# Kernel tuning notes

Measured on AMD Instinct MI355X. Metric: run time of the kernel, lower is better.

The kernel has to match this reference:

```python
import jax, jax.numpy as jnp
import numpy as np

GRID_SIZE = 100
N_GREEN = 524288
N_RED = 524288
LATENT_DIM = 10
HIDDEN = 128
IN_DIM = LATENT_DIM + 3 + 1  # z + level_data + loop index
TEMPERATURE = 500.0


def setup_inputs() -> dict:
    key = jax.random.key(0)
    ks = jax.random.split(key, 13)
    def lin(k, out_d, in_d):
        kw, kb = jax.random.split(k)
        s = 1.0 / np.sqrt(in_d)
        W = jax.random.uniform(kw, (out_d, in_d), jnp.float32, -s, s)
        b = jax.random.uniform(kb, (out_d,), jnp.float32, -s, s)
        return W, b
    z = jax.random.normal(ks[0], (LATENT_DIM,), jnp.float32)
    level_data = jnp.array([GRID_SIZE, N_GREEN, N_RED], dtype=jnp.int64)
    gW1, gb1 = lin(ks[1], HIDDEN, IN_DIM)
    gW2, gb2 = lin(ks[2], HIDDEN, HIDDEN)
    gW3, gb3 = lin(ks[3], 1, HIDDEN)
    rW1, rb1 = lin(ks[4], HIDDEN, IN_DIM)
    rW2, rb2 = lin(ks[5], HIDDEN, HIDDEN)
    rW3, rb3 = lin(ks[6], 1, HIDDEN)
    return {
        'z': z, 'level_data': level_data,
        'gW1': gW1, 'gb1': gb1, 'gW2': gW2, 'gb2': gb2, 'gW3': gW3, 'gb3': gb3,
        'rW1': rW1, 'rb1': rb1, 'rW2': rW2, 'rb2': rb2, 'rW3': rW3, 'rb3': rb3,
    }


def _mlp(x, W1, b1, W2, b2, W3, b3):
    # Linear -> LeakyReLU(0.2) -> Linear -> ELU(alpha=1) -> Linear
    h = jax.nn.leaky_relu(x @ W1.T + b1, negative_slope=0.2)
    h = jax.nn.elu(h @ W2.T + b2, alpha=1.0)
    return h @ W3.T + b3  # [N, 1]


def _coords(z_ext, n, W1, b1, W2, b2, W3, b3, scale):
    # batch all loop indices 0..n-1 into one GEMM call instead of n tiny launches
    idx = jnp.arange(n, dtype=jnp.float32)[:, None]            # [n, 1]
    x = jnp.concatenate(
        [jnp.broadcast_to(z_ext, (n, z_ext.shape[0])), idx], axis=1)  # [n, 14]
    out = _mlp(x, W1, b1, W2, b2, W3, b3)[:, 0]                 # [n]
    return (jax.nn.sigmoid(out / TEMPERATURE) * scale).astype(jnp.int32)


def reference(z, level_data, gW1, gb1, gW2, gb2, gW3, gb3,
              rW1, rb1, rW2, rb2, rW3, rb3):
    scale = level_data[0].astype(jnp.float32) ** 2 - 1.0  # grid_size^2 - 1
    z_ext = jnp.concatenate([z, level_data.astype(jnp.float32)])  # [13]
    coords_green = _coords(z_ext, N_GREEN, gW1, gb1, gW2, gb2, gW3, gb3, scale)
    coords_red = _coords(z_ext, N_RED, rW1, rb1, rW2, rb2, rW3, rb3, scale)
    return coords_green, coords_red
```

## Files before the change

kernel.cpp:

```cpp
#include <hip/hip_runtime.h>
#include <hip/hip_bf16.h>
#include <math.h>


#define HIDDEN 128
#define REGIONS 129
#define NEVT 512
#define CDSTRIDE (NEVT + 8)
#define WS_HDR 16
#define STS(g)      (WS_HDR + (g)*HIDDEN)
#define TIMES_OFF   (WS_HDR + 2*HIDDEN)
#define TIMES(g,r)  (TIMES_OFF + ((g)*REGIONS + (r))*NEVT)
#define CTAB_OFF    (TIMES_OFF + 2*REGIONS*NEVT)
#define CTAB(g,r)   (CTAB_OFF + ((g)*REGIONS + (r))*CDSTRIDE)
#define DTAB_OFF    (CTAB_OFF + 2*REGIONS*CDSTRIDE)
#define DTAB(g,r)   (DTAB_OFF + ((g)*REGIONS + (r))*CDSTRIDE)

__device__ __constant__ float TH[4] = {-4.f, -1.8f, -0.7f, 0.f};
__device__ __constant__ float PM[5] = {0.f, 0.0668106f, 0.3011695f, 0.7191639f, 1.f};
__device__ __constant__ float PQ[5] = {-1.f, -0.7144420f, -0.2925961f, 0.f, 0.f};

__global__ __launch_bounds__(512) void build_kernel(
    const float* __restrict__ z, const int* __restrict__ level,
    const float* __restrict__ gW1, const float* __restrict__ gb1,
    const float* __restrict__ gW2, const float* __restrict__ gb2,
    const float* __restrict__ gW3, const float* __restrict__ gb3,
    const float* __restrict__ rW1, const float* __restrict__ rb1,
    const float* __restrict__ rW2, const float* __restrict__ rb2,
    const float* __restrict__ rW3, const float* __restrict__ rb3,
    float* __restrict__ ws, int N)
{
    int g = blockIdx.x / REGIONS;
    int r = blockIdx.x - g * REGIONS;
    const float* W1 = g ? rW1 : gW1;  const float* b1 = g ? rb1 : gb1;
    const float* W2 = g ? rW2 : gW2;  const float* b2 = g ? rb2 : gb2;
    const float* W3 = g ? rW3 : gW3;  const float* b3 = g ? rb3 : gb3;

    __shared__ float zext[16];
    __shared__ float cs[HIDDEN], wv[HIDDEN], tb_l[HIDDEN], sts[HIDDEN];
    __shared__ float sc[HIDDEN], sw[HIDDEN], al[HIDDEN], be[HIDDEN];
    __shared__ float pa[4][HIDDEN], pb[4][HIDDEN];
    __shared__ float ev_t[NEVT], ev_c[NEVT], ev_d[NEVT];
    __shared__ float so_t[NEVT], so_c[NEVT], so_d[NEVT];
    __shared__ float pc_[NEVT], pd_[NEVT];
    __shared__ float c0s, d0s;
    __shared__ int cnt;
    int t = threadIdx.x;

    if (t == 0) {
        int g0 = level[0], l1 = level[1], l2 = level[2];
        if (l1 == 0) { l1 = level[2]; l2 = level[4]; }
        zext[10] = (float)g0; zext[11] = (float)l1; zext[12] = (float)l2;
        cnt = 0;
        if (blockIdx.x == 0) ws[0] = (float)g0 * (float)g0 - 1.0f;
    }
    if (t < 10) zext[t] = z[t];
    __syncthreads();

    if (t < HIDDEN) {
        float c = b1[t];
        #pragma unroll
        for (int q = 0; q < 13; ++q) c = fmaf(W1[t * 14 + q], zext[q], c);
        float w = W1[t * 14 + 13];
        cs[t] = c; wv[t] = w;
        float Nf = (float)N, tb = -c / w;
        if (!(tb > 0.0f)) tb = 0.0f;
        if (!(tb < Nf))  tb = Nf;
        tb_l[t] = tb;
    }
    __syncthreads();
    if (t < HIDDEN) {
        float tb = tb_l[t]; int rk = 0;
        for (int k = 0; k < HIDDEN; ++k) {
            float tk = tb_l[k];
            rk += (tk < tb || (tk == tb && k < t)) ? 1 : 0;
        }
        sts[rk] = tb;
        if (r == 0) ws[STS(g) + rk] = tb;
    }
    __syncthreads();
    float i0 = (r == 0) ? 0.0f : sts[r - 1];
    float i1 = (r == REGIONS - 1) ? (float)N : sts[r];

    if (t < HIDDEN) {
        float c = cs[t], w = wv[t];
        float mid = 0.5f * (i0 + i1);
        float s = (fmaf(mid, w, c) > 0.0f) ? 1.0f : 0.2f;
        sc[t] = s * c;  sw[t] = s * w;
    }
    __syncthreads();

    {
        int k = t & 127, q = t >> 7;
        float a = 0.0f, bb = 0.0f;
        const float4* row4 = (const float4*)(W2 + k * HIDDEN + q * 32);
        #pragma unroll
        for (int j4 = 0; j4 < 8; ++j4) {
            float4 w2 = row4[j4]; int j = q * 32 + j4 * 4;
            a = fmaf(w2.x, sc[j+0], a);  bb = fmaf(w2.x, sw[j+0], bb);
            a = fmaf(w2.y, sc[j+1], a);  bb = fmaf(w2.y, sw[j+1], bb);
            a = fmaf(w2.z, sc[j+2], a);  bb = fmaf(w2.z, sw[j+2], bb);
            a = fmaf(w2.w, sc[j+3], a);  bb = fmaf(w2.w, sw[j+3], bb);
        }
        pa[q][k] = a;  pb[q][k] = bb;
    }
    __syncthreads();
    if (t < HIDDEN) {
        al[t] = pa[0][t] + pa[1][t] + pa[2][t] + pa[3][t] + b2[t];
        be[t] = pb[0][t] + pb[1][t] + pb[2][t] + pb[3][t];
    }
    __syncthreads();

    {
        int ku = t >> 2, h = t & 3;
        float a = al[ku], b = be[ku], w3 = W3[ku];
        float p0 = fmaf(i0, b, a);
        int pcq = (p0 >= TH[0]) + (p0 >= TH[1]) + (p0 >= TH[2]) + (p0 >= TH[3]);
        bool up = (b > 0.0f), dn = (b < 0.0f);
        bool dir_ok = up ? (h >= pcq) : (dn && (h < pcq));
        float tc = (TH[h] - a) / b;
        if (dir_ok && (tc <= i1)) {
            float dm, dq;
            if (up) { dm = PM[h+1] - PM[h]; dq = PQ[h+1] - PQ[h]; }
            else    { dm = PM[h] - PM[h+1]; dq = PQ[h] - PQ[h+1]; }
            int pos = atomicAdd(&cnt, 1);
            ev_t[pos] = tc;
            ev_c[pos] = w3 * fmaf(dm, a, dq);
            ev_d[pos] = w3 * dm * b;
        }
    }
    if (t < HIDDEN) {
        float a = al[t], b = be[t], w3 = W3[t];
        float p0 = fmaf(i0, b, a);
        int pp = (p0 >= TH[0]) + (p0 >= TH[1]) + (p0 >= TH[2]) + (p0 >= TH[3]);
        pa[0][t] = w3 * fmaf(PM[pp], a, PQ[pp]);
        pb[0][t] = w3 * PM[pp] * b;
    }
    __syncthreads();
    int m = cnt;

    if (t < 64) {
        float sA = pa[0][t] + pa[0][t + 64];
        float sB = pb[0][t] + pb[0][t + 64];
        #pragma unroll
        for (int off = 32; off >= 1; off >>= 1) {
            sA += __shfl_down(sA, off);
            sB += __shfl_down(sB, off);
        }
        if (t == 0) { c0s = sA + b3[0]; d0s = sB; }
    }
    if (t < m) {
        float myt = ev_t[t]; int rk = 0;
        for (int e = 0; e < m; ++e) {
            float te = ev_t[e];
            rk += (te < myt || (te == myt && e < t)) ? 1 : 0;
        }
        so_t[rk] = myt;  so_c[rk] = ev_c[t];  so_d[rk] = ev_d[t];
    }
    __syncthreads();
    if (t < m) {
        float vc = 0.0f, vd = 0.0f;
        for (int e = 0; e <= t; ++e) { vc += so_c[e]; vd += so_d[e]; }
        pc_[t] = vc;  pd_[t] = vd;
    }
    __syncthreads();

    float C0 = c0s, D0 = d0s;
    float totc = (m > 0) ? pc_[m - 1] : 0.0f;
    float totd = (m > 0) ? pd_[m - 1] : 0.0f;
    float* Tt = ws + TIMES(g, r);
    float* Tc = ws + CTAB(g, r);
    float* Td = ws + DTAB(g, r);
    Tt[t]     = (t < m) ? so_t[t] : INFINITY;
    Tc[t + 1] = C0 + ((t < m) ? pc_[t] : totc);
    Td[t + 1] = D0 + ((t < m) ? pd_[t] : totd);
    if (t == 0) { Tc[0] = C0; Td[0] = D0; }
}

__device__ __forceinline__ void seg_lookup(
    const float* __restrict__ ws, const float* __restrict__ lts,
    int g, float fi, int& r, int& a)
{
    int lo = 0, hi = HIDDEN;
    #pragma unroll
    for (int s = 0; s < 7; ++s) { int mm = (lo + hi) >> 1; if (lts[mm] <= fi) lo = mm + 1; else hi = mm; }
    r = lo;
    const float* Tt = ws + TIMES(g, r);
    int aa = 0, bb = NEVT;
    #pragma unroll
    for (int s = 0; s < 9; ++s) { int mm = (aa + bb) >> 1; if (Tt[mm] <= fi) aa = mm + 1; else bb = mm; }
    a = aa;
}

__global__ __launch_bounds__(256) void gen_kernel(
    const float* __restrict__ ws, int* __restrict__ out, int N, int total)
{
    __shared__ float lts[HIDDEN];
    __shared__ float uC, uD, uScale;
    __shared__ int ra[2];
    int tid = threadIdx.x;
    int e0 = blockIdx.x * 256;
    int g = (e0 >= N) ? 1 : 0;
    int e = e0 + tid;
    if (tid < HIDDEN) lts[tid] = ws[STS(g) + tid];
    if (tid == 0) uScale = ws[0];
    __syncthreads();

    float fi = (float)(e - g * N);
    if (tid < 2) {
        float fq = (float)((tid == 0 ? e0 : e0 + 255) - g * N);
        int rr, aa; seg_lookup(ws, lts, g, fq, rr, aa);
        ra[tid] = (rr << 16) | aa;
        if (tid == 0) { uC = ws[CTAB(g, rr) + aa]; uD = ws[DTAB(g, rr) + aa]; }
    }
    __syncthreads();

    float C, D;
    if (ra[0] == ra[1]) {
        C = uC; D = uD;
    } else {
        int rr, aa; seg_lookup(ws, lts, g, fi, rr, aa);
        C = ws[CTAB(g, rr) + aa];
        D = ws[DTAB(g, rr) + aa];
    }
    float o = fmaf(fi, D, C);
    float sg = 1.0f / (1.0f + __expf(-o * (1.0f / 500.0f)));
    if (e < total) out[e] = (int)(sg * uScale);
}

extern "C" void kernel_launch(void* const* d_in, const int* in_sizes, int n_in,
                              void* d_out, int out_size, void* d_ws, size_t ws_size,
                              hipStream_t stream) {
    const float* z   = (const float*)d_in[0];
    const int* level = (const int*)d_in[1];
    const float* gW1 = (const float*)d_in[2];
    const float* gb1 = (const float*)d_in[3];
    const float* gW2 = (const float*)d_in[4];
    const float* gb2 = (const float*)d_in[5];
    const float* gW3 = (const float*)d_in[6];
    const float* gb3 = (const float*)d_in[7];
    const float* rW1 = (const float*)d_in[8];
    const float* rb1 = (const float*)d_in[9];
    const float* rW2 = (const float*)d_in[10];
    const float* rb2 = (const float*)d_in[11];
    const float* rW3 = (const float*)d_in[12];
    const float* rb3 = (const float*)d_in[13];
    int* out  = (int*)d_out;
    float* ws = (float*)d_ws;
    int N = out_size / 2;

    build_kernel<<<2 * REGIONS, 512, 0, stream>>>(z, level,
        gW1, gb1, gW2, gb2, gW3, gb3, rW1, rb1, rW2, rb2, rW3, rb3, ws, N);
    gen_kernel<<<(out_size + 255) / 256, 256, 0, stream>>>(ws, out, N, out_size);
}
```

Measured before the change: 97.28 us.

## Replace per-element binary search with chunk directory and vectorized sequential scan

The build kernel now writes a directory that maps each 128-element chunk to its starting region and event index, plus each region's end time. The gen kernel reads this directory entry and then advances linearly through events while producing four outputs per thread with an int4 store. This removes the two binary searches per element and the shared-memory setup in the gen kernel. The per-region prefix sum becomes a serial loop on one thread, and building the directory adds an O(m) count per chunk in the build kernel, which may lengthen it. The int4 store assumes the total output size is a multiple of four.

```diff
diff --git a/kernel.cpp b/kernel.cpp
--- a/kernel.cpp
+++ b/kernel.cpp
@@ -7,14 +7,17 @@
 #define REGIONS 129
 #define NEVT 512
 #define CDSTRIDE (NEVT + 8)
+#define CHUNK_SH 7
 #define WS_HDR 16
-#define STS(g)      (WS_HDR + (g)*HIDDEN)
-#define TIMES_OFF   (WS_HDR + 2*HIDDEN)
+#define TIMES_OFF   (WS_HDR)
 #define TIMES(g,r)  (TIMES_OFF + ((g)*REGIONS + (r))*NEVT)
 #define CTAB_OFF    (TIMES_OFF + 2*REGIONS*NEVT)
 #define CTAB(g,r)   (CTAB_OFF + ((g)*REGIONS + (r))*CDSTRIDE)
 #define DTAB_OFF    (CTAB_OFF + 2*REGIONS*CDSTRIDE)
 #define DTAB(g,r)   (DTAB_OFF + ((g)*REGIONS + (r))*CDSTRIDE)
+#define RTS_OFF     (DTAB_OFF + 2*REGIONS*CDSTRIDE)
+#define RTS(g)      (RTS_OFF + (g)*REGIONS)
+#define DIR_OFF     (RTS_OFF + 2*REGIONS + 16)
 
 __device__ __constant__ float TH[4] = {-4.f, -1.8f, -0.7f, 0.f};
 __device__ __constant__ float PM[5] = {0.f, 0.0668106f, 0.3011695f, 0.7191639f, 1.f};
@@ -28,7 +31,7 @@
     const float* __restrict__ rW1, const float* __restrict__ rb1,
     const float* __restrict__ rW2, const float* __restrict__ rb2,
     const float* __restrict__ rW3, const float* __restrict__ rb3,
-    float* __restrict__ ws, int N)
+    float* __restrict__ ws, int* __restrict__ dir, int N, int nchunk)
 {
     int g = blockIdx.x / REGIONS;
     int r = blockIdx.x - g * REGIONS;
@@ -41,8 +44,7 @@
     __shared__ float sc[HIDDEN], sw[HIDDEN], al[HIDDEN], be[HIDDEN];
     __shared__ float pa[4][HIDDEN], pb[4][HIDDEN];
     __shared__ float ev_t[NEVT], ev_c[NEVT], ev_d[NEVT];
-    __shared__ float so_t[NEVT], so_c[NEVT], so_d[NEVT];
-    __shared__ float pc_[NEVT], pd_[NEVT];
+    __shared__ float so_t[NEVT], pc_[NEVT], pd_[NEVT];
     __shared__ float c0s, d0s;
     __shared__ int cnt;
     int t = threadIdx.x;
@@ -76,11 +78,11 @@
             rk += (tk < tb || (tk == tb && k < t)) ? 1 : 0;
         }
         sts[rk] = tb;
-        if (r == 0) ws[STS(g) + rk] = tb;
     }
     __syncthreads();
     float i0 = (r == 0) ? 0.0f : sts[r - 1];
     float i1 = (r == REGIONS - 1) ? (float)N : sts[r];
+    if (t == 0) ws[RTS(g) + r] = i1;
 
     if (t < HIDDEN) {
         float c = cs[t], w = wv[t];
@@ -155,13 +157,12 @@
             float te = ev_t[e];
             rk += (te < myt || (te == myt && e < t)) ? 1 : 0;
         }
-        so_t[rk] = myt;  so_c[rk] = ev_c[t];  so_d[rk] = ev_d[t];
-    }
-    __syncthreads();
-    if (t < m) {
+        so_t[rk] = myt;  pc_[rk] = ev_c[t];  pd_[rk] = ev_d[t];
+    }
+    __syncthreads();
+    if (t == 0) {
         float vc = 0.0f, vd = 0.0f;
-        for (int e = 0; e <= t; ++e) { vc += so_c[e]; vd += so_d[e]; }
-        pc_[t] = vc;  pd_[t] = vd;
+        for (int e = 0; e < m; ++e) { vc += pc_[e]; vd += pd_[e]; pc_[e] = vc; pd_[e] = vd; }
     }
     __syncthreads();
 
@@ -175,57 +176,56 @@
     Tc[t + 1] = C0 + ((t < m) ? pc_[t] : totc);
     Td[t + 1] = D0 + ((t < m) ? pd_[t] : totd);
     if (t == 0) { Tc[0] = C0; Td[0] = D0; }
+
+    int qlo = ((int)i0) >> CHUNK_SH;
+    for (int q = qlo + t; ; q += 512) {
+        float fc = (float)(q << CHUNK_SH);
+        if (!(fc < i1)) break;
+        if (fc >= i0 && q < nchunk) {
+            int a = 0;
+            for (int e = 0; e < m; ++e) a += (so_t[e] <= fc) ? 1 : 0;
+            dir[g * nchunk + q] = (r << 16) | a;
+        }
+    }
 }
 
-__device__ __forceinline__ void seg_lookup(
-    const float* __restrict__ ws, const float* __restrict__ lts,
-    int g, float fi, int& r, int& a)
+__global__ __launch_bounds__(256) void gen_kernel(
+    const float* __restrict__ ws, const int* __restrict__ dir,
+    int* __restrict__ out, int N, int total, int nchunk)
 {
-    int lo = 0, hi = HIDDEN;
+    int e0 = (blockIdx.x * 256 + threadIdx.x) * 4;
+    if (e0 >= total) return;
+    int g = (e0 >= N) ? 1 : 0;
+    int i = e0 - g * N;
+
+    int pd = dir[g * nchunk + (i >> CHUNK_SH)];
+    int r = pd >> 16, a = pd & 0xffff;
+    const float* Tt = ws + TIMES(g, r);
+    const float* Tc = ws + CTAB(g, r);
+    const float* Td = ws + DTAB(g, r);
+    const float* RT = ws + RTS(g);
+    float rtEnd = RT[r];
+    float nextT = Tt[a];
+    float C = Tc[a], D = Td[a];
+    float scale = ws[0];
+
+    int4 res;
     #pragma unroll
-    for (int s = 0; s < 7; ++s) { int mm = (lo + hi) >> 1; if (lts[mm] <= fi) lo = mm + 1; else hi = mm; }
-    r = lo;
-    const float* Tt = ws + TIMES(g, r);
-    int aa = 0, bb = NEVT;
-    #pragma unroll
-    for (int s = 0; s < 9; ++s) { int mm = (aa + bb) >> 1; if (Tt[mm] <= fi) aa = mm + 1; else bb = mm; }
-    a = aa;
-}
-
-__global__ __launch_bounds__(256) void gen_kernel(
-    const float* __restrict__ ws, int* __restrict__ out, int N, int total)
-{
-    __shared__ float lts[HIDDEN];
-    __shared__ float uC, uD, uScale;
-    __shared__ int ra[2];
-    int tid = threadIdx.x;
-    int e0 = blockIdx.x * 256;
-    int g = (e0 >= N) ? 1 : 0;
-    int e = e0 + tid;
-    if (tid < HIDDEN) lts[tid] = ws[STS(g) + tid];
-    if (tid == 0) uScale = ws[0];
-    __syncthreads();
-
-    float fi = (float)(e - g * N);
-    if (tid < 2) {
-        float fq = (float)((tid == 0 ? e0 : e0 + 255) - g * N);
-        int rr, aa; seg_lookup(ws, lts, g, fq, rr, aa);
-        ra[tid] = (rr << 16) | aa;
-        if (tid == 0) { uC = ws[CTAB(g, rr) + aa]; uD = ws[DTAB(g, rr) + aa]; }
-    }
-    __syncthreads();
-
-    float C, D;
-    if (ra[0] == ra[1]) {
-        C = uC; D = uD;
-    } else {
-        int rr, aa; seg_lookup(ws, lts, g, fi, rr, aa);
-        C = ws[CTAB(g, rr) + aa];
-        D = ws[DTAB(g, rr) + aa];
-    }
-    float o = fmaf(fi, D, C);
-    float sg = 1.0f / (1.0f + __expf(-o * (1.0f / 500.0f)));
-    if (e < total) out[e] = (int)(sg * uScale);
+    for (int q = 0; q < 4; ++q) {
+        float fi = (float)(i + q);
+        while (fi >= rtEnd) {
+            ++r; a = 0;
+            Tt = ws + TIMES(g, r); Tc = ws + CTAB(g, r); Td = ws + DTAB(g, r);
+            rtEnd = RT[r]; nextT = Tt[0]; C = Tc[0]; D = Td[0];
+        }
+        while (nextT <= fi) {
+            ++a; nextT = Tt[a]; C = Tc[a]; D = Td[a];
+        }
+        float o = fmaf(fi, D, C);
+        float sg = 1.0f / (1.0f + __expf(-o * (1.0f / 500.0f)));
+        ((int*)&res)[q] = (int)(sg * scale);
+    }
+    ((int4*)out)[e0 >> 2] = res;
 }
 
 extern "C" void kernel_launch(void* const* d_in, const int* in_sizes, int n_in,
@@ -247,9 +247,13 @@
     const float* rb3 = (const float*)d_in[13];
     int* out  = (int*)d_out;
     float* ws = (float*)d_ws;
+    int* dir  = (int*)(ws + DIR_OFF);
     int N = out_size / 2;
+    int nchunk = (N + (1 << CHUNK_SH) - 1) >> CHUNK_SH;
 
     build_kernel<<<2 * REGIONS, 512, 0, stream>>>(z, level,
-        gW1, gb1, gW2, gb2, gW3, gb3, rW1, rb1, rW2, rb2, rW3, rb3, ws, N);
-    gen_kernel<<<(out_size + 255) / 256, 256, 0, stream>>>(ws, out, N, out_size);
+        gW1, gb1, gW2, gb2, gW3, gb3, rW1, rb1, rW2, rb2, rW3, rb3,
+        ws, dir, N, nchunk);
+    gen_kernel<<<(out_size / 4 + 255) / 256, 256, 0, stream>>>(ws, dir, out,
+                                                               N, out_size, nchunk);
 }
```

Measured after the change: 93.06 us. -4.3%, faster.
